# Kernel tuning notes

Hardware: AMD Instinct MI355X
Metric: run time of the kernel (lower is better)

Reference implementation:

```python
import jax, jax.numpy as jnp
import numpy as np

EMBED_DIM = 256
NUM_HEADS = 8
PROJ_DIM = EMBED_DIM // NUM_HEADS


def setup_inputs() -> dict:
    key = jax.random.key(0)
    ks = jax.random.split(key, 5)
    scale = 1.0 / np.sqrt(EMBED_DIM)
    inputs = jax.random.normal(ks[0], (2, 12, 12, 12, EMBED_DIM), dtype=jnp.float32)
    Wq = jax.random.normal(ks[1], (EMBED_DIM, EMBED_DIM), dtype=jnp.float32) * scale
    Wk = jax.random.normal(ks[2], (EMBED_DIM, EMBED_DIM), dtype=jnp.float32) * scale
    Wv = jax.random.normal(ks[3], (EMBED_DIM, EMBED_DIM), dtype=jnp.float32) * scale
    Wo = jax.random.normal(ks[4], (EMBED_DIM, EMBED_DIM), dtype=jnp.float32) * scale
    z = jnp.zeros((EMBED_DIM,), dtype=jnp.float32)
    return {"inputs": inputs, "Wq": Wq, "bq": z, "Wk": Wk, "bk": z,
            "Wv": Wv, "bv": z, "Wo": Wo, "bo": z}


def reference(inputs, Wq, bq, Wk, bk, Wv, bv, Wo, bo):
    B, h, w, d, E = inputs.shape
    S = h * w * d  # flattened spatial sequence
    x = inputs.reshape(B, S, E)
    # projections + head split: [B, S, E] -> [B, H, S, P]
    def split_heads(t):
        return t.reshape(B, S, NUM_HEADS, PROJ_DIM).transpose(0, 2, 1, 3)
    q = split_heads(x @ Wq + bq)
    k = split_heads(x @ Wk + bk)
    v = split_heads(x @ Wv + bv)
    # NOTE: original module does NOT scale by 1/sqrt(proj_dim)
    scores = jnp.einsum('bhsp,bhtp->bhst', q, k)  # [B, H, S, S]
    attn = jax.nn.softmax(scores, axis=-1)
    out = jnp.einsum('bhst,bhtp->bhsp', attn, v)  # [B, H, S, P]
    out = out.transpose(0, 2, 1, 3).reshape(B, h, w, d, E)
    return out @ Wo + bo
```

## Files before the change

### kernel.cpp

```cpp
#include <hip/hip_runtime.h>
#include <math.h>

#define EMBED 256
#define HEADS 8
#define PDIM  32
#define BATCH 2
#define SEQ   1728
#define NTOK  (BATCH*SEQ)
#define NE    (NTOK*EMBED)
#define LOG2E 1.44269504088896f

typedef __attribute__((ext_vector_type(8))) __bf16 bf16x8;
typedef __attribute__((ext_vector_type(4))) float  f32x4;
typedef unsigned short ushort_t;
typedef unsigned int   uint_t;

static __device__ __forceinline__ unsigned short f2bf_rne(float f) {
    union { float f; unsigned u; } x; x.f = f;
    unsigned r = x.u + 0x7fffu + ((x.u >> 16) & 1u);
    return (unsigned short)(r >> 16);
}
union v8cast { uint4 u; bf16x8 v; };

static __device__ __forceinline__ void cvt8_hilo(const float f[8], bf16x8& hi, bf16x8& lo) {
    uint4 ph, pl;
    uint_t* phv = (uint_t*)&ph; uint_t* plv = (uint_t*)&pl;
    #pragma unroll
    for (int j = 0; j < 4; ++j) {
        const float f0 = f[2 * j], f1 = f[2 * j + 1];
        const uint_t u0 = __float_as_uint(f0) + 0x8000u;
        const uint_t u1 = __float_as_uint(f1) + 0x8000u;
        phv[j] = __builtin_amdgcn_perm(u1, u0, 0x07060302u);
        const float l0 = f0 - __uint_as_float(u0 & 0xFFFF0000u);
        const float l1 = f1 - __uint_as_float(u1 & 0xFFFF0000u);
        plv[j] = __builtin_amdgcn_perm(__float_as_uint(l1) + 0x8000u,
                                       __float_as_uint(l0) + 0x8000u, 0x07060302u);
    }
    v8cast ch; ch.u = ph; hi = ch.v;
    v8cast cl; cl.u = pl; lo = cl.v;
}

__global__ __launch_bounds__(64) void qkv_gemm_kernel(
    const float* __restrict__ x,
    const float* __restrict__ Wq, const float* __restrict__ bq,
    const float* __restrict__ Wk, const float* __restrict__ bk,
    const float* __restrict__ Wv, const float* __restrict__ bv,
    ushort_t* __restrict__ qo, ushort_t* __restrict__ ko, ushort_t* __restrict__ vt)
{
    const int lane = threadIdx.x, li = lane & 15, quad = lane >> 4;
    const int m0 = blockIdx.x * 64, n0 = blockIdx.y * 32, z = blockIdx.z;
    const float* __restrict__ W    = (z == 0) ? Wq : (z == 1) ? Wk : Wv;
    const float* __restrict__ bias = (z == 0) ? bq : (z == 1) ? bk : bv;

    const float* ap = x + (size_t)(m0 + li) * EMBED + quad * 8;

    f32x4 acc[4][2];
    #pragma unroll
    for (int mt = 0; mt < 4; ++mt)
        #pragma unroll
        for (int nt = 0; nt < 2; ++nt)
            acc[mt][nt] = (f32x4){0.f, 0.f, 0.f, 0.f};

    #pragma unroll 2
    for (int k0 = 0; k0 < EMBED; k0 += 32) {
        bf16x8 ah[4], al[4];
        #pragma unroll
        for (int mt = 0; mt < 4; ++mt) {
            float af[8];
            *(float4*)&af[0] = *(const float4*)(ap + (size_t)mt * 16 * EMBED + k0);
            *(float4*)&af[4] = *(const float4*)(ap + (size_t)mt * 16 * EMBED + k0 + 4);
            cvt8_hilo(af, ah[mt], al[mt]);
        }
        bf16x8 bh[2], bl[2];
        #pragma unroll
        for (int nt = 0; nt < 2; ++nt) {
            const int n = n0 + nt * 16 + li;
            const float* wp = W + (size_t)(k0 + quad * 8) * EMBED + n;
            float bf[8];
            #pragma unroll
            for (int jj = 0; jj < 8; ++jj) bf[jj] = wp[(size_t)jj * EMBED];
            cvt8_hilo(bf, bh[nt], bl[nt]);
        }
        #pragma unroll
        for (int mt = 0; mt < 4; ++mt)
            #pragma unroll
            for (int nt = 0; nt < 2; ++nt) {
                acc[mt][nt] = __builtin_amdgcn_mfma_f32_16x16x32_bf16(ah[mt], bh[nt], acc[mt][nt], 0, 0, 0);
                acc[mt][nt] = __builtin_amdgcn_mfma_f32_16x16x32_bf16(al[mt], bh[nt], acc[mt][nt], 0, 0, 0);
                acc[mt][nt] = __builtin_amdgcn_mfma_f32_16x16x32_bf16(ah[mt], bl[nt], acc[mt][nt], 0, 0, 0);
            }
    }

    const int b = m0 / SEQ;
    const int sbase = m0 - b * SEQ;

    if (z <= 1) {
        ushort_t* __restrict__ dst = z ? ko : qo;
        #pragma unroll
        for (int nt = 0; nt < 2; ++nt) {
            const int gcol = n0 + nt * 16 + li;
            const int h = gcol >> 5, p = gcol & 31;
            const float bb = bias[gcol];
            ushort_t* base = dst + ((size_t)(b * HEADS + h) * SEQ) * PDIM + p;
            #pragma unroll
            for (int mt = 0; mt < 4; ++mt)
                #pragma unroll
                for (int r = 0; r < 4; ++r) {
                    const int s = sbase + mt * 16 + quad * 4 + r;
                    base[(size_t)s * PDIM] = f2bf_rne(acc[mt][nt][r] + bb);
                }
        }
    } else {
        #pragma unroll
        for (int nt = 0; nt < 2; ++nt) {
            const int gcol = n0 + nt * 16 + li;
            const int h = gcol >> 5, p = gcol & 31;
            const float bb = bias[gcol];
            ushort_t* base = vt + ((size_t)(b * HEADS + h) * PDIM + p) * SEQ;
            #pragma unroll
            for (int mt = 0; mt < 4; ++mt) {
                const int s0 = sbase + mt * 16 + quad * 4;
                ushort4 wv4;
                wv4.x = f2bf_rne(acc[mt][nt][0] + bb);
                wv4.y = f2bf_rne(acc[mt][nt][1] + bb);
                wv4.z = f2bf_rne(acc[mt][nt][2] + bb);
                wv4.w = f2bf_rne(acc[mt][nt][3] + bb);
                *(ushort4*)&base[s0] = wv4;
            }
        }
    }
}

__global__ __launch_bounds__(256) void attn_kernel(
    const ushort_t* __restrict__ q, const ushort_t* __restrict__ k,
    const ushort_t* __restrict__ vt, ushort_t* __restrict__ aob)
{
    const int t    = threadIdx.x;
    const int lane = t & 63, w = t >> 6;
    const int li   = lane & 15, quad = lane >> 4;
    const int pr   = w >> 1;
    const int c    = w & 1;
    const int bh = blockIdx.y;
    const int b  = bh >> 3, h = bh & 7;
    const int q0 = blockIdx.x * 32 + pr * 16;

    const ushort_t* __restrict__ qb = q  + (size_t)bh * SEQ * PDIM;
    const ushort_t* __restrict__ kb = k  + (size_t)bh * SEQ * PDIM;
    const ushort_t* __restrict__ vb = vt + (size_t)bh * PDIM * SEQ;

    __shared__ ushort_t Ks[2][64][40];
    __shared__ ushort_t Vs[2][32][72];
    __shared__ ushort_t Ps[4][16][72];
    __shared__ float OS[2][16][32];
    __shared__ float mS[2][16], lS[2][16];

    const bf16x8 qfrag = *(const bf16x8*)(qb + (size_t)(q0 + li) * PDIM + quad * 8);

    const int jk = pr * 32 + (lane >> 1), ck = (lane & 1) * 8;
    const int pv = pr * 16 + (lane >> 2), cv = (lane & 3) * 8;
    const ushort_t* kgp = kb + (size_t)jk * PDIM + ck;
    const ushort_t* vgp = vb + (size_t)pv * SEQ + cv;

    f32x4 o0 = {0.f, 0.f, 0.f, 0.f};
    f32x4 o1 = {0.f, 0.f, 0.f, 0.f};
    float m_run = -__builtin_inff(), l_run = 0.f;

    const int kt0 = c ? 13 : 0;

    uint4 kr0 = *(const uint4*)(kgp + (size_t)kt0 * 64 * PDIM);
    uint4 kr1 = *(const uint4*)(kgp + (size_t)kt0 * 64 * PDIM + 16);
    uint4 vr0 = *(const uint4*)(vgp + kt0 * 64);
    uint4 vr1 = *(const uint4*)(vgp + kt0 * 64 + 32);

    for (int it = 0; it < 14; ++it) {
        __syncthreads();
        *(uint4*)&Ks[c][jk][ck]      = kr0;
        *(uint4*)&Ks[c][jk][ck + 16] = kr1;
        *(uint4*)&Vs[c][pv][cv]      = vr0;
        *(uint4*)&Vs[c][pv][cv + 32] = vr1;
        __syncthreads();
        if (it + 1 < 14) {
            const int tn = kt0 + it + 1;
            kr0 = *(const uint4*)(kgp + (size_t)tn * 64 * PDIM);
            kr1 = *(const uint4*)(kgp + (size_t)tn * 64 * PDIM + 16);
            vr0 = *(const uint4*)(vgp + tn * 64);
            vr1 = *(const uint4*)(vgp + tn * 64 + 32);
        }

        if (c == 0 || it > 0) {
            const f32x4 zero = {0.f, 0.f, 0.f, 0.f};
            f32x4 st[4];
            #pragma unroll
            for (int jt = 0; jt < 4; ++jt) {
                const bf16x8 kf = *(const bf16x8*)&Ks[c][jt * 16 + li][quad * 8];
                st[jt] = __builtin_amdgcn_mfma_f32_16x16x32_bf16(kf, qfrag, zero, 0, 0, 0);
            }

            float tm = st[0][0];
            #pragma unroll
            for (int jt = 0; jt < 4; ++jt)
                #pragma unroll
                for (int r = 0; r < 4; ++r) tm = fmaxf(tm, st[jt][r]);
            tm = fmaxf(tm, __shfl_xor(tm, 16));
            tm = fmaxf(tm, __shfl_xor(tm, 32));
            const float mnew  = fmaxf(m_run, tm);
            const float negml = -(mnew * LOG2E);

            float ps = 0.f;
            #pragma unroll
            for (int jt = 0; jt < 4; ++jt) {
                const float p0 = __builtin_amdgcn_exp2f(fmaf(st[jt][0], LOG2E, negml));
                const float p1 = __builtin_amdgcn_exp2f(fmaf(st[jt][1], LOG2E, negml));
                const float p2 = __builtin_amdgcn_exp2f(fmaf(st[jt][2], LOG2E, negml));
                const float p3 = __builtin_amdgcn_exp2f(fmaf(st[jt][3], LOG2E, negml));
                ps += (p0 + p1) + (p2 + p3);
                uint2 pw;
                pw.x = __builtin_amdgcn_perm(__float_as_uint(p1) + 0x8000u,
                                             __float_as_uint(p0) + 0x8000u, 0x07060302u);
                pw.y = __builtin_amdgcn_perm(__float_as_uint(p3) + 0x8000u,
                                             __float_as_uint(p2) + 0x8000u, 0x07060302u);
                *(uint2*)&Ps[w][li][16 * jt + 4 * quad] = pw;
            }
            ps += __shfl_xor(ps, 16);
            ps += __shfl_xor(ps, 32);

            const float alpha = __builtin_amdgcn_exp2f(fmaf(m_run, LOG2E, negml));
            l_run = fmaf(l_run, alpha, ps);
            m_run = mnew;

            float af[4];
            #pragma unroll
            for (int r = 0; r < 4; ++r) af[r] = __shfl(alpha, 4 * quad + r);
            #pragma unroll
            for (int r = 0; r < 4; ++r) { o0[r] *= af[r]; o1[r] *= af[r]; }

            const bf16x8 pa0 = *(const bf16x8*)&Ps[w][li][8 * quad];
            const bf16x8 pa1 = *(const bf16x8*)&Ps[w][li][32 + 8 * quad];
            const bf16x8 vf00 = *(const bf16x8*)&Vs[c][li][quad * 8];
            const bf16x8 vf01 = *(const bf16x8*)&Vs[c][16 + li][quad * 8];
            const bf16x8 vf10 = *(const bf16x8*)&Vs[c][li][32 + quad * 8];
            const bf16x8 vf11 = *(const bf16x8*)&Vs[c][16 + li][32 + quad * 8];
            o0 = __builtin_amdgcn_mfma_f32_16x16x32_bf16(pa0, vf00, o0, 0, 0, 0);
            o0 = __builtin_amdgcn_mfma_f32_16x16x32_bf16(pa1, vf10, o0, 0, 0, 0);
            o1 = __builtin_amdgcn_mfma_f32_16x16x32_bf16(pa0, vf01, o1, 0, 0, 0);
            o1 = __builtin_amdgcn_mfma_f32_16x16x32_bf16(pa1, vf11, o1, 0, 0, 0);
        }
    }

    __syncthreads();
    if (c == 1) {
        if (quad == 0) { mS[pr][li] = m_run; lS[pr][li] = l_run; }
        #pragma unroll
        for (int r = 0; r < 4; ++r) {
            OS[pr][4 * quad + r][li]      = o0[r];
            OS[pr][4 * quad + r][16 + li] = o1[r];
        }
    }
    __syncthreads();
    if (c == 0) {
        const float m1 = mS[pr][li], l1 = lS[pr][li];
        const float M  = fmaxf(m_run, m1);
        const float a0 = __builtin_amdgcn_exp2f((m_run - M) * LOG2E);
        const float a1 = __builtin_amdgcn_exp2f((m1    - M) * LOG2E);
        const float lt = a0 * l_run + a1 * l1;
        #pragma unroll
        for (int r = 0; r < 4; ++r) {
            const int row = 4 * quad + r;
            const float af0  = __shfl(a0, row);
            const float af1  = __shfl(a1, row);
            const float linv = 1.0f / __shfl(lt, row);
            const float v0 = (af0 * o0[r] + af1 * OS[pr][row][li])      * linv;
            const float v1 = (af0 * o1[r] + af1 * OS[pr][row][16 + li]) * linv;
            const int s = q0 + row;
            ushort_t* orow = aob + ((size_t)(b * SEQ + s)) * EMBED + h * PDIM;
            orow[li]      = f2bf_rne(v0);
            orow[16 + li] = f2bf_rne(v1);
        }
    }
}

__global__ __launch_bounds__(64) void out_gemm_kernel(
    const ushort_t* __restrict__ a, const float* __restrict__ Wo,
    const float* __restrict__ bo, float* __restrict__ out)
{
    const int lane = threadIdx.x, li = lane & 15, quad = lane >> 4;
    const int m0 = blockIdx.x * 64, n0 = blockIdx.y * 16;

    const ushort_t* aph = a + (size_t)(m0 + li) * EMBED + quad * 8;

    f32x4 acc[4];
    #pragma unroll
    for (int mt = 0; mt < 4; ++mt) acc[mt] = (f32x4){0.f, 0.f, 0.f, 0.f};

    #pragma unroll 2
    for (int k0 = 0; k0 < EMBED; k0 += 32) {
        bf16x8 ah[4];
        #pragma unroll
        for (int mt = 0; mt < 4; ++mt)
            ah[mt] = *(const bf16x8*)(aph + (size_t)mt * 16 * EMBED + k0);
        const float* wp = Wo + (size_t)(k0 + quad * 8) * EMBED + n0 + li;
        uint4 pb;
        uint_t* pbv = (uint_t*)&pb;
        #pragma unroll
        for (int j = 0; j < 4; ++j) {
            const uint_t u0 = __float_as_uint(wp[(size_t)(2 * j) * EMBED])     + 0x8000u;
            const uint_t u1 = __float_as_uint(wp[(size_t)(2 * j + 1) * EMBED]) + 0x8000u;
            pbv[j] = __builtin_amdgcn_perm(u1, u0, 0x07060302u);
        }
        v8cast cb; cb.u = pb;
        #pragma unroll
        for (int mt = 0; mt < 4; ++mt)
            acc[mt] = __builtin_amdgcn_mfma_f32_16x16x32_bf16(ah[mt], cb.v, acc[mt], 0, 0, 0);
    }

    const float bb = bo[n0 + li];
    #pragma unroll
    for (int mt = 0; mt < 4; ++mt)
        #pragma unroll
        for (int r = 0; r < 4; ++r) {
            const int row = m0 + mt * 16 + quad * 4 + r;
            out[(size_t)row * EMBED + n0 + li] = acc[mt][r] + bb;
        }
}

extern "C" void kernel_launch(void* const* d_in, const int* in_sizes, int n_in,
                              void* d_out, int out_size, void* d_ws, size_t ws_size,
                              hipStream_t stream)
{
    const float* x  = (const float*)d_in[0];
    const float* Wq = (const float*)d_in[1];
    const float* bq = (const float*)d_in[2];
    const float* Wk = (const float*)d_in[3];
    const float* bk = (const float*)d_in[4];
    const float* Wv = (const float*)d_in[5];
    const float* bv = (const float*)d_in[6];
    const float* Wo = (const float*)d_in[7];
    const float* bo = (const float*)d_in[8];
    float* out = (float*)d_out;

    ushort_t* ws = (ushort_t*)d_ws;
    ushort_t* qg = ws;
    ushort_t* kg = qg + (size_t)NE;
    ushort_t* vg = kg + (size_t)NE;
    ushort_t* ag = vg + (size_t)NE;

    qkv_gemm_kernel<<<dim3(54, 8, 3), 64, 0, stream>>>(
        x, Wq, bq, Wk, bk, Wv, bv, qg, kg, vg);
    attn_kernel<<<dim3(54, 16), 256, 0, stream>>>(qg, kg, vg, ag);
    out_gemm_kernel<<<dim3(54, 16), 64, 0, stream>>>(ag, Wo, bo, out);
}
```

Before: 121.7 us.

## Stage converted weight tiles in LDS shared by four waves in QKV and output GEMMs

Both projection GEMMs now run four waves per block. Each block converts its weight column slice to bf16 (hi/lo split for QKV) once into shared memory, and all waves then read it from there. Before, each wave did strided global loads and the conversion itself. This cuts redundant weight traffic and conversion work, in exchange for fewer, larger blocks (14 along M, with the tail waves idle) and a barrier. The rows are padded to reduce LDS bank conflicts.

```diff
diff --git a/kernel.cpp b/kernel.cpp
--- a/kernel.cpp
+++ b/kernel.cpp
@@ -9,6 +9,7 @@
 #define NTOK  (BATCH*SEQ)
 #define NE    (NTOK*EMBED)
 #define LOG2E 1.44269504088896f
+#define BROW  266
 
 typedef __attribute__((ext_vector_type(8))) __bf16 bf16x8;
 typedef __attribute__((ext_vector_type(4))) float  f32x4;
@@ -40,17 +41,45 @@
     v8cast cl; cl.u = pl; lo = cl.v;
 }
 
-__global__ __launch_bounds__(64) void qkv_gemm_kernel(
+__global__ __launch_bounds__(256) void qkv_gemm_kernel(
     const float* __restrict__ x,
     const float* __restrict__ Wq, const float* __restrict__ bq,
     const float* __restrict__ Wk, const float* __restrict__ bk,
     const float* __restrict__ Wv, const float* __restrict__ bv,
     ushort_t* __restrict__ qo, ushort_t* __restrict__ ko, ushort_t* __restrict__ vt)
 {
-    const int lane = threadIdx.x, li = lane & 15, quad = lane >> 4;
-    const int m0 = blockIdx.x * 64, n0 = blockIdx.y * 32, z = blockIdx.z;
+    const int t    = threadIdx.x;
+    const int lane = t & 63, w = t >> 6;
+    const int li   = lane & 15, quad = lane >> 4;
+    const int m0 = blockIdx.x * 256 + w * 64;
+    const int n0 = blockIdx.y * 32, z = blockIdx.z;
     const float* __restrict__ W    = (z == 0) ? Wq : (z == 1) ? Wk : Wv;
     const float* __restrict__ bias = (z == 0) ? bq : (z == 1) ? bk : bv;
+
+    __shared__ ushort_t BsH[32][BROW];
+    __shared__ ushort_t BsL[32][BROW];
+
+    {
+        const int n  = t & 31;
+        const int kc = (t >> 5) * 32;
+        const float* wp = W + (size_t)kc * EMBED + n0 + n;
+        ushort_t hv[32], lv[32];
+        #pragma unroll
+        for (int kk = 0; kk < 32; ++kk) {
+            const float v  = wp[(size_t)kk * EMBED];
+            const uint_t u = __float_as_uint(v) + 0x8000u;
+            hv[kk] = (ushort_t)(u >> 16);
+            lv[kk] = f2bf_rne(v - __uint_as_float(u & 0xFFFF0000u));
+        }
+        #pragma unroll
+        for (int c = 0; c < 4; ++c) {
+            *(uint4*)&BsH[n][kc + c * 8] = *(uint4*)&hv[c * 8];
+            *(uint4*)&BsL[n][kc + c * 8] = *(uint4*)&lv[c * 8];
+        }
+    }
+    __syncthreads();
+
+    if (m0 >= NTOK) return;
 
     const float* ap = x + (size_t)(m0 + li) * EMBED + quad * 8;
 
@@ -74,12 +103,8 @@
         bf16x8 bh[2], bl[2];
         #pragma unroll
         for (int nt = 0; nt < 2; ++nt) {
-            const int n = n0 + nt * 16 + li;
-            const float* wp = W + (size_t)(k0 + quad * 8) * EMBED + n;
-            float bf[8];
-            #pragma unroll
-            for (int jj = 0; jj < 8; ++jj) bf[jj] = wp[(size_t)jj * EMBED];
-            cvt8_hilo(bf, bh[nt], bl[nt]);
+            bh[nt] = *(const bf16x8*)&BsH[nt * 16 + li][k0 + quad * 8];
+            bl[nt] = *(const bf16x8*)&BsL[nt * 16 + li][k0 + quad * 8];
         }
         #pragma unroll
         for (int mt = 0; mt < 4; ++mt)
@@ -279,12 +304,32 @@
     }
 }
 
-__global__ __launch_bounds__(64) void out_gemm_kernel(
+__global__ __launch_bounds__(256) void out_gemm_kernel(
     const ushort_t* __restrict__ a, const float* __restrict__ Wo,
     const float* __restrict__ bo, float* __restrict__ out)
 {
-    const int lane = threadIdx.x, li = lane & 15, quad = lane >> 4;
-    const int m0 = blockIdx.x * 64, n0 = blockIdx.y * 16;
+    const int t    = threadIdx.x;
+    const int lane = t & 63, w = t >> 6;
+    const int li   = lane & 15, quad = lane >> 4;
+    const int m0 = blockIdx.x * 256 + w * 64;
+    const int n0 = blockIdx.y * 16;
+
+    __shared__ ushort_t BsH[16][BROW];
+
+    {
+        const int n  = t & 15;
+        const int kc = (t >> 4) * 16;
+        const float* wp = Wo + (size_t)kc * EMBED + n0 + n;
+        ushort_t hv[16];
+        #pragma unroll
+        for (int kk = 0; kk < 16; ++kk)
+            hv[kk] = f2bf_rne(wp[(size_t)kk * EMBED]);
+        *(uint4*)&BsH[n][kc]     = *(uint4*)&hv[0];
+        *(uint4*)&BsH[n][kc + 8] = *(uint4*)&hv[8];
+    }
+    __syncthreads();
+
+    if (m0 >= NTOK) return;
 
     const ushort_t* aph = a + (size_t)(m0 + li) * EMBED + quad * 8;
 
@@ -298,19 +343,10 @@
         #pragma unroll
         for (int mt = 0; mt < 4; ++mt)
             ah[mt] = *(const bf16x8*)(aph + (size_t)mt * 16 * EMBED + k0);
-        const float* wp = Wo + (size_t)(k0 + quad * 8) * EMBED + n0 + li;
-        uint4 pb;
-        uint_t* pbv = (uint_t*)&pb;
-        #pragma unroll
-        for (int j = 0; j < 4; ++j) {
-            const uint_t u0 = __float_as_uint(wp[(size_t)(2 * j) * EMBED])     + 0x8000u;
-            const uint_t u1 = __float_as_uint(wp[(size_t)(2 * j + 1) * EMBED]) + 0x8000u;
-            pbv[j] = __builtin_amdgcn_perm(u1, u0, 0x07060302u);
-        }
-        v8cast cb; cb.u = pb;
+        const bf16x8 bh = *(const bf16x8*)&BsH[li][k0 + quad * 8];
         #pragma unroll
         for (int mt = 0; mt < 4; ++mt)
-            acc[mt] = __builtin_amdgcn_mfma_f32_16x16x32_bf16(ah[mt], cb.v, acc[mt], 0, 0, 0);
+            acc[mt] = __builtin_amdgcn_mfma_f32_16x16x32_bf16(ah[mt], bh, acc[mt], 0, 0, 0);
     }
 
     const float bb = bo[n0 + li];
@@ -344,8 +380,8 @@
     ushort_t* vg = kg + (size_t)NE;
     ushort_t* ag = vg + (size_t)NE;
 
-    qkv_gemm_kernel<<<dim3(54, 8, 3), 64, 0, stream>>>(
+    qkv_gemm_kernel<<<dim3(14, 8, 3), 256, 0, stream>>>(
         x, Wq, bq, Wk, bk, Wv, bv, qg, kg, vg);
     attn_kernel<<<dim3(54, 16), 256, 0, stream>>>(qg, kg, vg, ag);
-    out_gemm_kernel<<<dim3(54, 16), 64, 0, stream>>>(ag, Wo, bo, out);
-}
+    out_gemm_kernel<<<dim3(14, 16), 256, 0, stream>>>(ag, Wo, bo, out);
+}
```

New measurement: 125.1 us. 1.03x slower.

## Load attention K/V fragments straight from global into registers, drop LDS staging

Applied to the files above, without the earlier changes.

The attention kernel drops from four waves to two per block. Each wave now handles both 16-row query groups and reads K and V MFMA fragments directly from global memory into registers, double-buffered across tiles, instead of staging them through shared memory with two barriers per tile. This removes the LDS copies and block-wide syncs in the main loop, and each loaded K/V fragment is reused for two query groups. In exchange it uses more registers, issues less coalesced global loads that rely on cache, and changes launch-bounds occupancy hints on all three kernels.

```diff
diff --git a/kernel.cpp b/kernel.cpp
--- a/kernel.cpp
+++ b/kernel.cpp
@@ -40,7 +40,7 @@
     v8cast cl; cl.u = pl; lo = cl.v;
 }
 
-__global__ __launch_bounds__(64) void qkv_gemm_kernel(
+__global__ __launch_bounds__(64, 2) void qkv_gemm_kernel(
     const float* __restrict__ x,
     const float* __restrict__ Wq, const float* __restrict__ bq,
     const float* __restrict__ Wk, const float* __restrict__ bk,
@@ -131,70 +131,63 @@
     }
 }
 
-__global__ __launch_bounds__(256) void attn_kernel(
+__global__ __launch_bounds__(128, 3) void attn_kernel(
     const ushort_t* __restrict__ q, const ushort_t* __restrict__ k,
     const ushort_t* __restrict__ vt, ushort_t* __restrict__ aob)
 {
     const int t    = threadIdx.x;
-    const int lane = t & 63, w = t >> 6;
+    const int lane = t & 63;
+    const int c    = t >> 6;
     const int li   = lane & 15, quad = lane >> 4;
-    const int pr   = w >> 1;
-    const int c    = w & 1;
     const int bh = blockIdx.y;
     const int b  = bh >> 3, h = bh & 7;
-    const int q0 = blockIdx.x * 32 + pr * 16;
+    const int q0 = blockIdx.x * 32;
 
     const ushort_t* __restrict__ qb = q  + (size_t)bh * SEQ * PDIM;
     const ushort_t* __restrict__ kb = k  + (size_t)bh * SEQ * PDIM;
     const ushort_t* __restrict__ vb = vt + (size_t)bh * PDIM * SEQ;
 
-    __shared__ ushort_t Ks[2][64][40];
-    __shared__ ushort_t Vs[2][32][72];
-    __shared__ ushort_t Ps[4][16][72];
+    __shared__ ushort_t Ps[2][2][16][72];
     __shared__ float OS[2][16][32];
     __shared__ float mS[2][16], lS[2][16];
 
-    const bf16x8 qfrag = *(const bf16x8*)(qb + (size_t)(q0 + li) * PDIM + quad * 8);
-
-    const int jk = pr * 32 + (lane >> 1), ck = (lane & 1) * 8;
-    const int pv = pr * 16 + (lane >> 2), cv = (lane & 3) * 8;
-    const ushort_t* kgp = kb + (size_t)jk * PDIM + ck;
-    const ushort_t* vgp = vb + (size_t)pv * SEQ + cv;
-
-    f32x4 o0 = {0.f, 0.f, 0.f, 0.f};
-    f32x4 o1 = {0.f, 0.f, 0.f, 0.f};
-    float m_run = -__builtin_inff(), l_run = 0.f;
-
-    const int kt0 = c ? 13 : 0;
-
-    uint4 kr0 = *(const uint4*)(kgp + (size_t)kt0 * 64 * PDIM);
-    uint4 kr1 = *(const uint4*)(kgp + (size_t)kt0 * 64 * PDIM + 16);
-    uint4 vr0 = *(const uint4*)(vgp + kt0 * 64);
-    uint4 vr1 = *(const uint4*)(vgp + kt0 * 64 + 32);
-
-    for (int it = 0; it < 14; ++it) {
-        __syncthreads();
-        *(uint4*)&Ks[c][jk][ck]      = kr0;
-        *(uint4*)&Ks[c][jk][ck + 16] = kr1;
-        *(uint4*)&Vs[c][pv][cv]      = vr0;
-        *(uint4*)&Vs[c][pv][cv + 32] = vr1;
-        __syncthreads();
-        if (it + 1 < 14) {
-            const int tn = kt0 + it + 1;
-            kr0 = *(const uint4*)(kgp + (size_t)tn * 64 * PDIM);
-            kr1 = *(const uint4*)(kgp + (size_t)tn * 64 * PDIM + 16);
-            vr0 = *(const uint4*)(vgp + tn * 64);
-            vr1 = *(const uint4*)(vgp + tn * 64 + 32);
-        }
-
-        if (c == 0 || it > 0) {
-            const f32x4 zero = {0.f, 0.f, 0.f, 0.f};
+    bf16x8 qfrag[2];
+    #pragma unroll
+    for (int g = 0; g < 2; ++g)
+        qfrag[g] = *(const bf16x8*)(qb + (size_t)(q0 + g * 16 + li) * PDIM + quad * 8);
+
+    const ushort_t* kptr = kb + (size_t)li * PDIM + quad * 8;
+    const ushort_t* vptr = vb + (size_t)li * SEQ + quad * 8;
+
+    f32x4 o[2][2];
+    #pragma unroll
+    for (int g = 0; g < 2; ++g) { o[g][0] = (f32x4){0,0,0,0}; o[g][1] = (f32x4){0,0,0,0}; }
+    float m_run[2] = {-__builtin_inff(), -__builtin_inff()};
+    float l_run[2] = {0.f, 0.f};
+
+    bf16x8 kf0[4], vf0[4], kf1[4], vf1[4];
+
+#define LOAD_TILE(KF, VF, J0) do {                                           \
+        const ushort_t* kp = kptr + (size_t)(J0) * PDIM;                     \
+        KF[0] = *(const bf16x8*)(kp);                                        \
+        KF[1] = *(const bf16x8*)(kp + 16 * PDIM);                            \
+        KF[2] = *(const bf16x8*)(kp + 32 * PDIM);                            \
+        KF[3] = *(const bf16x8*)(kp + 48 * PDIM);                            \
+        const ushort_t* vp = vptr + (J0);                                    \
+        VF[0] = *(const bf16x8*)(vp);                    \
+        VF[1] = *(const bf16x8*)(vp + 16 * SEQ);         \
+        VF[2] = *(const bf16x8*)(vp + 32);              \
+        VF[3] = *(const bf16x8*)(vp + 32 + 16 * SEQ);   \
+    } while (0)
+
+    auto compute_tile = [&](const bf16x8* kf, const bf16x8* vf) {
+        const f32x4 zero = {0.f, 0.f, 0.f, 0.f};
+        #pragma unroll
+        for (int g = 0; g < 2; ++g) {
             f32x4 st[4];
             #pragma unroll
-            for (int jt = 0; jt < 4; ++jt) {
-                const bf16x8 kf = *(const bf16x8*)&Ks[c][jt * 16 + li][quad * 8];
-                st[jt] = __builtin_amdgcn_mfma_f32_16x16x32_bf16(kf, qfrag, zero, 0, 0, 0);
-            }
+            for (int jt = 0; jt < 4; ++jt)
+                st[jt] = __builtin_amdgcn_mfma_f32_16x16x32_bf16(kf[jt], qfrag[g], zero, 0, 0, 0);
 
             float tm = st[0][0];
             #pragma unroll
@@ -203,7 +196,7 @@
                 for (int r = 0; r < 4; ++r) tm = fmaxf(tm, st[jt][r]);
             tm = fmaxf(tm, __shfl_xor(tm, 16));
             tm = fmaxf(tm, __shfl_xor(tm, 32));
-            const float mnew  = fmaxf(m_run, tm);
+            const float mnew  = fmaxf(m_run[g], tm);
             const float negml = -(mnew * LOG2E);
 
             float ps = 0.f;
@@ -219,67 +212,82 @@
                                              __float_as_uint(p0) + 0x8000u, 0x07060302u);
                 pw.y = __builtin_amdgcn_perm(__float_as_uint(p3) + 0x8000u,
                                              __float_as_uint(p2) + 0x8000u, 0x07060302u);
-                *(uint2*)&Ps[w][li][16 * jt + 4 * quad] = pw;
+                *(uint2*)&Ps[c][g][li][16 * jt + 4 * quad] = pw;
             }
             ps += __shfl_xor(ps, 16);
             ps += __shfl_xor(ps, 32);
 
-            const float alpha = __builtin_amdgcn_exp2f(fmaf(m_run, LOG2E, negml));
-            l_run = fmaf(l_run, alpha, ps);
-            m_run = mnew;
+            const float alpha = __builtin_amdgcn_exp2f(fmaf(m_run[g], LOG2E, negml));
+            l_run[g] = fmaf(l_run[g], alpha, ps);
+            m_run[g] = mnew;
 
             float af[4];
             #pragma unroll
             for (int r = 0; r < 4; ++r) af[r] = __shfl(alpha, 4 * quad + r);
             #pragma unroll
-            for (int r = 0; r < 4; ++r) { o0[r] *= af[r]; o1[r] *= af[r]; }
-
-            const bf16x8 pa0 = *(const bf16x8*)&Ps[w][li][8 * quad];
-            const bf16x8 pa1 = *(const bf16x8*)&Ps[w][li][32 + 8 * quad];
-            const bf16x8 vf00 = *(const bf16x8*)&Vs[c][li][quad * 8];
-            const bf16x8 vf01 = *(const bf16x8*)&Vs[c][16 + li][quad * 8];
-            const bf16x8 vf10 = *(const bf16x8*)&Vs[c][li][32 + quad * 8];
-            const bf16x8 vf11 = *(const bf16x8*)&Vs[c][16 + li][32 + quad * 8];
-            o0 = __builtin_amdgcn_mfma_f32_16x16x32_bf16(pa0, vf00, o0, 0, 0, 0);
-            o0 = __builtin_amdgcn_mfma_f32_16x16x32_bf16(pa1, vf10, o0, 0, 0, 0);
-            o1 = __builtin_amdgcn_mfma_f32_16x16x32_bf16(pa0, vf01, o1, 0, 0, 0);
-            o1 = __builtin_amdgcn_mfma_f32_16x16x32_bf16(pa1, vf11, o1, 0, 0, 0);
-        }
-    }
-
-    __syncthreads();
+            for (int r = 0; r < 4; ++r) { o[g][0][r] *= af[r]; o[g][1][r] *= af[r]; }
+
+            const bf16x8 pa0 = *(const bf16x8*)&Ps[c][g][li][8 * quad];
+            const bf16x8 pa1 = *(const bf16x8*)&Ps[c][g][li][32 + 8 * quad];
+            o[g][0] = __builtin_amdgcn_mfma_f32_16x16x32_bf16(pa0, vf[0], o[g][0], 0, 0, 0);
+            o[g][0] = __builtin_amdgcn_mfma_f32_16x16x32_bf16(pa1, vf[2], o[g][0], 0, 0, 0);
+            o[g][1] = __builtin_amdgcn_mfma_f32_16x16x32_bf16(pa0, vf[1], o[g][1], 0, 0, 0);
+            o[g][1] = __builtin_amdgcn_mfma_f32_16x16x32_bf16(pa1, vf[3], o[g][1], 0, 0, 0);
+        }
+    };
+
+    const int jstart = c ? 896 : 0;
+    const int ntl    = c ? 13 : 14;
+
+    LOAD_TILE(kf0, vf0, jstart);
+    for (int kt = 0; kt < ntl; kt += 2) {
+        if (kt + 1 < ntl) LOAD_TILE(kf1, vf1, jstart + (kt + 1) * 64);
+        compute_tile(kf0, vf0);
+        if (kt + 1 < ntl) {
+            if (kt + 2 < ntl) LOAD_TILE(kf0, vf0, jstart + (kt + 2) * 64);
+            compute_tile(kf1, vf1);
+        }
+    }
+#undef LOAD_TILE
+
     if (c == 1) {
-        if (quad == 0) { mS[pr][li] = m_run; lS[pr][li] = l_run; }
-        #pragma unroll
-        for (int r = 0; r < 4; ++r) {
-            OS[pr][4 * quad + r][li]      = o0[r];
-            OS[pr][4 * quad + r][16 + li] = o1[r];
+        #pragma unroll
+        for (int g = 0; g < 2; ++g) {
+            if (quad == 0) { mS[g][li] = m_run[g]; lS[g][li] = l_run[g]; }
+            #pragma unroll
+            for (int r = 0; r < 4; ++r) {
+                OS[g][4 * quad + r][li]      = o[g][0][r];
+                OS[g][4 * quad + r][16 + li] = o[g][1][r];
+            }
         }
     }
     __syncthreads();
     if (c == 0) {
-        const float m1 = mS[pr][li], l1 = lS[pr][li];
-        const float M  = fmaxf(m_run, m1);
-        const float a0 = __builtin_amdgcn_exp2f((m_run - M) * LOG2E);
-        const float a1 = __builtin_amdgcn_exp2f((m1    - M) * LOG2E);
-        const float lt = a0 * l_run + a1 * l1;
-        #pragma unroll
-        for (int r = 0; r < 4; ++r) {
-            const int row = 4 * quad + r;
-            const float af0  = __shfl(a0, row);
-            const float af1  = __shfl(a1, row);
-            const float linv = 1.0f / __shfl(lt, row);
-            const float v0 = (af0 * o0[r] + af1 * OS[pr][row][li])      * linv;
-            const float v1 = (af0 * o1[r] + af1 * OS[pr][row][16 + li]) * linv;
-            const int s = q0 + row;
-            ushort_t* orow = aob + ((size_t)(b * SEQ + s)) * EMBED + h * PDIM;
-            orow[li]      = f2bf_rne(v0);
-            orow[16 + li] = f2bf_rne(v1);
-        }
-    }
-}
-
-__global__ __launch_bounds__(64) void out_gemm_kernel(
+        #pragma unroll
+        for (int g = 0; g < 2; ++g) {
+            const float m1 = mS[g][li], l1 = lS[g][li];
+            const float M  = fmaxf(m_run[g], m1);
+            const float a0 = __builtin_amdgcn_exp2f((m_run[g] - M) * LOG2E);
+            const float a1 = __builtin_amdgcn_exp2f((m1       - M) * LOG2E);
+            const float lt = a0 * l_run[g] + a1 * l1;
+            #pragma unroll
+            for (int r = 0; r < 4; ++r) {
+                const int row = 4 * quad + r;
+                const float af0  = __shfl(a0, row);
+                const float af1  = __shfl(a1, row);
+                const float linv = 1.0f / __shfl(lt, row);
+                const float v0 = (af0 * o[g][0][r] + af1 * OS[g][row][li])      * linv;
+                const float v1 = (af0 * o[g][1][r] + af1 * OS[g][row][16 + li]) * linv;
+                const int s = q0 + g * 16 + row;
+                ushort_t* orow = aob + ((size_t)(b * SEQ + s)) * EMBED + h * PDIM;
+                orow[li]      = f2bf_rne(v0);
+                orow[16 + li] = f2bf_rne(v1);
+            }
+        }
+    }
+}
+
+__global__ __launch_bounds__(64, 4) void out_gemm_kernel(
     const ushort_t* __restrict__ a, const float* __restrict__ Wo,
     const float* __restrict__ bo, float* __restrict__ out)
 {
@@ -346,6 +354,6 @@
 
     qkv_gemm_kernel<<<dim3(54, 8, 3), 64, 0, stream>>>(
         x, Wq, bq, Wk, bk, Wv, bv, qg, kg, vg);
-    attn_kernel<<<dim3(54, 16), 256, 0, stream>>>(qg, kg, vg, ag);
+    attn_kernel<<<dim3(54, 16), 128, 0, stream>>>(qg, kg, vg, ag);
     out_gemm_kernel<<<dim3(54, 16), 64, 0, stream>>>(ag, Wo, bo, out);
 }
```

After: 123.9 us. About the same (+1.8%).
